# Performance work log

Hardware: AMD Instinct MI355X
Metric: run time of the kernel (lower is better)

The kernel has to match this reference:

```python
import jax, jax.numpy as jnp
import numpy as np

N_HEAD = 16
TEMPERATURE = 1.0

def setup_inputs() -> dict:
    key = jax.random.key(0)
    ks = jax.random.split(key, 5)
    B, L, D = 2, 2048, 1024
    s = 0.02
    return {
        'x':     jax.random.normal(ks[0], (B, L, D), jnp.float32),
        'q_g':   jax.random.normal(ks[1], (B, L, D), jnp.float32),
        'k_g':   jax.random.normal(ks[2], (B, L, D), jnp.float32),
        'W_qkv': jax.random.normal(ks[3], (D, 3 * D), jnp.float32) * s,
        'W_out': jax.random.normal(ks[4], (D, D), jnp.float32) * s,
    }

def reference(x, q_g, k_g, W_qkv, W_out):
    B, L, D = x.shape
    H = N_HEAD
    hd = D // H
    qkv = x @ W_qkv                                    # [B, L, 3D]
    q, k, v = jnp.split(qkv, 3, axis=-1)
    def to_heads(t):                                    # [B,L,D] -> [B,H,L,hd]
        return t.reshape(B, L, H, hd).transpose(0, 2, 1, 3)
    q, k, v = to_heads(q), to_heads(k), to_heads(v)
    qg, kg = to_heads(q_g), to_heads(k_g)

    scale = 1.0 / jnp.sqrt(jnp.float32(hd))
    # dual score matrices (same math as concat-on-head-dim then split)
    aw_x = jnp.einsum('bhqd,bhkd->bhqk', q, k) * scale    # [B,H,L,L]
    aw_g = jnp.einsum('bhqd,bhkd->bhqk', qg, kg) * scale  # [B,H,L,L]
    # sensory_attention=True, merge='add'
    attn = aw_x + aw_g

    causal = jnp.tril(jnp.ones((L, L), dtype=bool))
    attn = jnp.where(causal, attn, -jnp.inf)
    log_norm = jnp.log(jnp.float32(L))                    # softmax_log_norm=True
    attn = jax.nn.softmax(attn / (log_norm * TEMPERATURE), axis=-1)

    y = jnp.einsum('bhqk,bhkd->bhqd', attn, v)            # [B,H,L,hd]
    y = y.transpose(0, 2, 1, 3).reshape(B, L, D)
    return y @ W_out
```

## Files before the change

kernel.cpp:

```cpp
#include <hip/hip_runtime.h>
#include <type_traits>

typedef __attribute__((ext_vector_type(8))) short bf16x8;
typedef __attribute__((ext_vector_type(4))) float f32x4;

static __device__ __forceinline__ unsigned short f2bf(float f) {
    unsigned int u = __float_as_uint(f);
    u += 0x7fffu + ((u >> 16) & 1u);
    return (unsigned short)(u >> 16);
}
static __device__ __forceinline__ unsigned short f2bf_fast(float f) {
    return (unsigned short)((__float_as_uint(f) + 0x8000u) >> 16);
}

static __device__ __forceinline__ float bf2f(short v) {
    return __uint_as_float(((unsigned int)(unsigned short)v) << 16);
}

static __device__ __forceinline__ bf16x8 cvt8v(const float* p) {
    f32x4 a = *(const f32x4*)p, b = *(const f32x4*)(p + 4);
    bf16x8 r;
    r[0] = (short)f2bf(a[0]); r[1] = (short)f2bf(a[1]);
    r[2] = (short)f2bf(a[2]); r[3] = (short)f2bf(a[3]);
    r[4] = (short)f2bf(b[0]); r[5] = (short)f2bf(b[1]);
    r[6] = (short)f2bf(b[2]); r[7] = (short)f2bf(b[3]);
    return r;
}
static __device__ __forceinline__ bf16x8 scale8v(bf16x8 v, float s) {
    bf16x8 r;
    #pragma unroll
    for (int j = 0; j < 8; ++j) r[j] = (short)f2bf(bf2f(v[j]) * s);
    return r;
}
static __device__ __forceinline__ uint4 cvt8(const float* p) {
    bf16x8 r = cvt8v(p);
    union { bf16x8 v; uint4 u; } c; c.v = r; return c.u;
}

static __device__ __forceinline__ void glds16(const unsigned short* g, unsigned short* l) {
    __builtin_amdgcn_global_load_lds(
        (const __attribute__((address_space(1))) unsigned int*)g,
        (__attribute__((address_space(3))) unsigned int*)l, 16, 0, 0);
}

__global__ __launch_bounds__(256) void cvt_bf16(
    const float* __restrict__ src, unsigned short* __restrict__ dst, int n8)
{
    int i = blockIdx.x * 256 + threadIdx.x;
    if (i < n8) *(uint4*)&dst[(size_t)i * 8] = cvt8(&src[(size_t)i * 8]);
}

__global__ __launch_bounds__(256) void transpose_cvt(
    const float* __restrict__ src, unsigned short* __restrict__ dst, int R, int C)
{
    __shared__ unsigned short t[64 * 72];
    const int r0 = blockIdx.y * 64, c0 = blockIdx.x * 64;
    const int tid = threadIdx.x;
    #pragma unroll
    for (int i = 0; i < 4; ++i) {
        int idx = tid + i * 256;
        int row = idx >> 4, seg = idx & 15;
        f32x4 v = *(const f32x4*)&src[(size_t)(r0 + row) * C + c0 + seg * 4];
        #pragma unroll
        for (int j = 0; j < 4; ++j) t[row * 72 + seg * 4 + j] = f2bf(v[j]);
    }
    __syncthreads();
    #pragma unroll
    for (int i = 0; i < 2; ++i) {
        int idx = tid + i * 256;
        int row = idx >> 3, seg = idx & 7;
        uint4 tv; unsigned short* tmp = (unsigned short*)&tv;
        #pragma unroll
        for (int j = 0; j < 8; ++j) tmp[j] = t[(seg * 8 + j) * 72 + row];
        *(uint4*)&dst[(size_t)(c0 + row) * R + r0 + seg * 8] = tv;
    }
}

__global__ __launch_bounds__(256) void transpose_v(
    const unsigned short* __restrict__ qkv, unsigned short* __restrict__ vt)
{
    __shared__ unsigned short t[64 * 72];
    const int lt = blockIdx.x, bh = blockIdx.y, b = bh >> 4, h = bh & 15;
    const int tid = threadIdx.x;
    #pragma unroll
    for (int i = 0; i < 2; ++i) {
        int idx = tid + i * 256, row = idx >> 3, seg = idx & 7;
        *(uint4*)&t[row * 72 + seg * 8] =
            *(const uint4*)&qkv[(size_t)(b * 2048 + lt * 64 + row) * 3072 + 2048 + h * 64 + seg * 8];
    }
    __syncthreads();
    #pragma unroll
    for (int i = 0; i < 2; ++i) {
        int idx = tid + i * 256, row = idx >> 3, seg = idx & 7;
        uint4 tv; unsigned short* tmp = (unsigned short*)&tv;
        #pragma unroll
        for (int j = 0; j < 8; ++j) tmp[j] = t[(seg * 8 + j) * 72 + row];
        *(uint4*)&vt[((size_t)bh * 64 + row) * 2048 + lt * 64 + seg * 8] = tv;
    }
}

template <typename OT>
__global__ __launch_bounds__(256) void gemm_lds(
    const unsigned short* __restrict__ A, const unsigned short* __restrict__ Bt,
    OT* __restrict__ C, int M, int N, int K)
{
    __shared__ unsigned short As[128 * 32];
    __shared__ unsigned short Bs[128 * 32];
    const int tid = threadIdx.x;
    const int wave = tid >> 6, lane = tid & 63, quad = lane >> 4, l16 = lane & 15;
    const int wr = (wave >> 1) * 64, wc = (wave & 1) * 64;
    const int m0 = blockIdx.y * 128, n0 = blockIdx.x * 128;

    const unsigned short* ga = A  + (size_t)(m0 + wave * 32 + (lane >> 2)) * K + (lane & 3) * 8;
    const unsigned short* gb = Bt + (size_t)(n0 + wave * 32 + (lane >> 2)) * K + (lane & 3) * 8;
    unsigned short* la = &As[wave * 32 * 32];
    unsigned short* lb = &Bs[wave * 32 * 32];
    const size_t step16 = (size_t)16 * K;

    f32x4 acc[4][4];
    #pragma unroll
    for (int i = 0; i < 4; ++i)
        #pragma unroll
        for (int j = 0; j < 4; ++j) acc[i][j] = (f32x4){0.f, 0.f, 0.f, 0.f};

    for (int kt = 0; kt < K; kt += 32) {
        glds16(ga, la);
        glds16(ga + step16, la + 512);
        glds16(gb, lb);
        glds16(gb + step16, lb + 512);
        ga += 32; gb += 32;
        __syncthreads();
        bf16x8 af[4], bf[4];
        #pragma unroll
        for (int i = 0; i < 4; ++i) {
            af[i] = *(const bf16x8*)&As[(wr + i * 16 + l16) * 32 + quad * 8];
            bf[i] = *(const bf16x8*)&Bs[(wc + i * 16 + l16) * 32 + quad * 8];
        }
        #pragma unroll
        for (int mi = 0; mi < 4; ++mi)
            #pragma unroll
            for (int ni = 0; ni < 4; ++ni)
                acc[mi][ni] = __builtin_amdgcn_mfma_f32_16x16x32_bf16(
                    af[mi], bf[ni], acc[mi][ni], 0, 0, 0);
        __syncthreads();
    }
    #pragma unroll
    for (int mi = 0; mi < 4; ++mi)
        #pragma unroll
        for (int ni = 0; ni < 4; ++ni)
            #pragma unroll
            for (int r = 0; r < 4; ++r) {
                int row = m0 + wr + mi * 16 + quad * 4 + r;
                int col = n0 + wc + ni * 16 + l16;
                if constexpr (std::is_same_v<OT, float>)
                    C[(size_t)row * N + col] = acc[mi][ni][r];
                else
                    C[(size_t)row * N + col] = f2bf(acc[mi][ni][r]);
            }
}

__global__ __launch_bounds__(256, 4) void attn5(
    const unsigned short* __restrict__ qkv, const float* __restrict__ qg,
    const unsigned short* __restrict__ kgb, const unsigned short* __restrict__ vt,
    unsigned short* __restrict__ y)
{
    const int L = 2048, D3 = 3072, Dm = 1024;
    const float SC2 = 0.125f * 1.44269504088896f / 7.6246189861593985f;

    const int qt = 31 - (int)blockIdx.y;
    const int bh = blockIdx.x, b = bh >> 4, h = bh & 15;
    const int tid = threadIdx.x, wave = tid >> 6, lane = tid & 63;
    const int quad = lane >> 4, l16 = lane & 15;

    __shared__ unsigned short K_l[4096];
    __shared__ unsigned short G_l[4096];
    __shared__ unsigned short V_l[4096];
    __shared__ unsigned short P_l[4 * 1152];
    unsigned short* Pw = &P_l[wave * 1152];

    bf16x8 qf[2], gf[2];
    {
        const int qrow = qt * 64 + wave * 16 + l16;
        const unsigned short* qp = qkv + (size_t)(b * L + qrow) * D3 + h * 64;
        const float* gp = qg + (size_t)(b * L + qrow) * Dm + h * 64;
        #pragma unroll
        for (int c = 0; c < 2; ++c) {
            qf[c] = scale8v(*(const bf16x8*)(qp + c * 32 + quad * 8), SC2);
            gf[c] = scale8v(cvt8v(gp + c * 32 + quad * 8), SC2);
        }
    }

    f32x4 o[4];
    #pragma unroll
    for (int nd = 0; nd < 4; ++nd) o[nd] = (f32x4){0.f, 0.f, 0.f, 0.f};
    float lsum[4];
    #pragma unroll
    for (int r = 0; r < 4; ++r) lsum[r] = 0.f;

    const int srow = wave * 16 + (lane >> 3);
    const int c8 = (((lane & 7) ^ (lane >> 3)) & 7) * 8;
    const unsigned short* pk = qkv + (size_t)(b * L + srow) * D3 + 1024 + h * 64 + c8;
    const unsigned short* pg = kgb + (size_t)(b * L + srow) * Dm + h * 64 + c8;
    const unsigned short* pv = vt + ((size_t)bh * 64 + srow) * L + c8;
    unsigned short* lK = &K_l[wave * 1024];
    unsigned short* lG = &G_l[wave * 1024];
    unsigned short* lV = &V_l[wave * 1024];

    const int rb = l16 * 128;
    const int swz0 = ((quad     ^ (l16 & 7)) * 16);
    const int swz1 = (((4 + quad) ^ (l16 & 7)) * 16);

    const int ktmax = qt;
    for (int kt = 0; kt <= ktmax; ++kt) {
        __syncthreads();
        glds16(pk, lK); glds16(pk + 8 * D3, lK + 512);
        glds16(pg, lG); glds16(pg + 8 * Dm, lG + 512);
        glds16(pv, lV); glds16(pv + 8 * L,  lV + 512);
        pk += 64 * D3; pg += 64 * Dm; pv += 64;
        __syncthreads();

        f32x4 s[4];
        #pragma unroll
        for (int ni = 0; ni < 4; ++ni) {
            bf16x8 kf0 = *(const bf16x8*)((const char*)K_l + rb + swz0 + ni * 2048);
            bf16x8 kf1 = *(const bf16x8*)((const char*)K_l + rb + swz1 + ni * 2048);
            bf16x8 gb0 = *(const bf16x8*)((const char*)G_l + rb + swz0 + ni * 2048);
            bf16x8 gb1 = *(const bf16x8*)((const char*)G_l + rb + swz1 + ni * 2048);
            f32x4 a = (f32x4){0.f, 0.f, 0.f, 0.f};
            a = __builtin_amdgcn_mfma_f32_16x16x32_bf16(qf[0], kf0, a, 0, 0, 0);
            a = __builtin_amdgcn_mfma_f32_16x16x32_bf16(gf[0], gb0, a, 0, 0, 0);
            a = __builtin_amdgcn_mfma_f32_16x16x32_bf16(qf[1], kf1, a, 0, 0, 0);
            a = __builtin_amdgcn_mfma_f32_16x16x32_bf16(gf[1], gb1, a, 0, 0, 0);
            s[ni] = a;
        }

        {
            const int rowbase = qt * 64 + wave * 16 + quad * 4;
            const bool safe = (kt * 64 + 63 <= rowbase);
            #pragma unroll
            for (int ni = 0; ni < 4; ++ni) {
                const int key = kt * 64 + ni * 16 + l16;
                #pragma unroll
                for (int r = 0; r < 4; ++r) {
                    float e = (safe || key <= rowbase + r) ? exp2f(s[ni][r]) : 0.f;
                    lsum[r] += e;
                    Pw[(quad * 4 + r) * 72 + ni * 16 + l16] = f2bf_fast(e);
                }
            }
        }
        asm volatile("s_waitcnt lgkmcnt(0)" ::: "memory");

        bf16x8 pa[2];
        #pragma unroll
        for (int c = 0; c < 2; ++c)
            pa[c] = *(const bf16x8*)&Pw[l16 * 72 + c * 32 + quad * 8];
        #pragma unroll
        for (int nd = 0; nd < 4; ++nd) {
            bf16x8 vf0 = *(const bf16x8*)((const char*)V_l + rb + swz0 + nd * 2048);
            bf16x8 vf1 = *(const bf16x8*)((const char*)V_l + rb + swz1 + nd * 2048);
            o[nd] = __builtin_amdgcn_mfma_f32_16x16x32_bf16(pa[0], vf0, o[nd], 0, 0, 0);
            o[nd] = __builtin_amdgcn_mfma_f32_16x16x32_bf16(pa[1], vf1, o[nd], 0, 0, 0);
        }
    }

    #pragma unroll
    for (int r = 0; r < 4; ++r) {
        float rs = lsum[r];
        #pragma unroll
        for (int off = 1; off < 16; off <<= 1) rs += __shfl_xor(rs, off);
        float inv = 1.f / rs;
        int row = qt * 64 + wave * 16 + quad * 4 + r;
        #pragma unroll
        for (int nd = 0; nd < 4; ++nd)
            y[(size_t)(b * L + row) * Dm + h * 64 + nd * 16 + l16] =
                f2bf(o[nd][r] * inv);
    }
}

extern "C" void kernel_launch(void* const* d_in, const int* in_sizes, int n_in,
                              void* d_out, int out_size, void* d_ws, size_t ws_size,
                              hipStream_t stream) {
    const float* x     = (const float*)d_in[0];
    const float* q_g   = (const float*)d_in[1];
    const float* k_g   = (const float*)d_in[2];
    const float* W_qkv = (const float*)d_in[3];
    const float* W_out = (const float*)d_in[4];
    float* out = (float*)d_out;
    unsigned short* ws = (unsigned short*)d_ws;

    unsigned short* qkv_ws = ws;
    unsigned short* y_ws   = ws + 12582912;
    unsigned short* wtq    = ws + 16777216;
    unsigned short* wto    = ws + 19922944;
    unsigned short* kg_bf  = ws + 20971520;
    unsigned short* x_bf   = ws + 25165824;
    unsigned short* vt_bf  = x_bf;

    dim3 blk(256);
    cvt_bf16<<<2048, blk, 0, stream>>>(x,   x_bf,  524288);
    cvt_bf16<<<2048, blk, 0, stream>>>(k_g, kg_bf, 524288);
    transpose_cvt<<<dim3(48, 16), blk, 0, stream>>>(W_qkv, wtq, 1024, 3072);
    transpose_cvt<<<dim3(16, 16), blk, 0, stream>>>(W_out, wto, 1024, 1024);
    gemm_lds<unsigned short><<<dim3(24, 32), blk, 0, stream>>>(
        x_bf, wtq, qkv_ws, 4096, 3072, 1024);
    transpose_v<<<dim3(32, 32), blk, 0, stream>>>(qkv_ws, vt_bf);
    attn5<<<dim3(32, 32), blk, 0, stream>>>(qkv_ws, q_g, kg_bf, vt_bf, y_ws);
    gemm_lds<float><<<dim3(8, 32), blk, 0, stream>>>(
        y_ws, wto, out, 4096, 1024, 1024);
}
```

Before: 235.2 us.

## Peel diagonal tile, transpose score MFMA, pack P stores, merge convert launches

```diff
diff --git a/kernel.cpp b/kernel.cpp
--- a/kernel.cpp
+++ b/kernel.cpp
@@ -9,8 +9,9 @@
     u += 0x7fffu + ((u >> 16) & 1u);
     return (unsigned short)(u >> 16);
 }
-static __device__ __forceinline__ unsigned short f2bf_fast(float f) {
-    return (unsigned short)((__float_as_uint(f) + 0x8000u) >> 16);
+static __device__ __forceinline__ unsigned int pack2bf(float lo, float hi) {
+    return ((__float_as_uint(lo) + 0x8000u) >> 16) |
+           ((__float_as_uint(hi) + 0x8000u) & 0xffff0000u);
 }
 
 static __device__ __forceinline__ float bf2f(short v) {
@@ -43,11 +44,15 @@
         (__attribute__((address_space(3))) unsigned int*)l, 16, 0, 0);
 }
 
-__global__ __launch_bounds__(256) void cvt_bf16(
-    const float* __restrict__ src, unsigned short* __restrict__ dst, int n8)
+__global__ __launch_bounds__(256) void cvt_bf16_2(
+    const float* __restrict__ a, unsigned short* __restrict__ da,
+    const float* __restrict__ b, unsigned short* __restrict__ db)
 {
     int i = blockIdx.x * 256 + threadIdx.x;
-    if (i < n8) *(uint4*)&dst[(size_t)i * 8] = cvt8(&src[(size_t)i * 8]);
+    const float* s = (i < 524288) ? a : b;
+    unsigned short* d = (i < 524288) ? da : db;
+    size_t j = (size_t)((i < 524288) ? i : i - 524288) * 8;
+    *(uint4*)&d[j] = cvt8(&s[j]);
 }
 
 __global__ __launch_bounds__(256) void transpose_cvt(
@@ -159,7 +164,7 @@
             }
 }
 
-__global__ __launch_bounds__(256, 4) void attn5(
+__global__ __launch_bounds__(256, 4) void attn6(
     const unsigned short* __restrict__ qkv, const float* __restrict__ qg,
     const unsigned short* __restrict__ kgb, const unsigned short* __restrict__ vt,
     unsigned short* __restrict__ y)
@@ -193,9 +198,7 @@
     f32x4 o[4];
     #pragma unroll
     for (int nd = 0; nd < 4; ++nd) o[nd] = (f32x4){0.f, 0.f, 0.f, 0.f};
-    float lsum[4];
-    #pragma unroll
-    for (int r = 0; r < 4; ++r) lsum[r] = 0.f;
+    float lsum = 0.f;
 
     const int srow = wave * 16 + (lane >> 3);
     const int c8 = (((lane & 7) ^ (lane >> 3)) & 7) * 8;
@@ -210,8 +213,7 @@
     const int swz0 = ((quad     ^ (l16 & 7)) * 16);
     const int swz1 = (((4 + quad) ^ (l16 & 7)) * 16);
 
-    const int ktmax = qt;
-    for (int kt = 0; kt <= ktmax; ++kt) {
+    for (int kt = 0; kt < qt; ++kt) {
         __syncthreads();
         glds16(pk, lK); glds16(pk + 8 * D3, lK + 512);
         glds16(pg, lG); glds16(pg + 8 * Dm, lG + 512);
@@ -219,7 +221,6 @@
         pk += 64 * D3; pg += 64 * Dm; pv += 64;
         __syncthreads();
 
-        f32x4 s[4];
         #pragma unroll
         for (int ni = 0; ni < 4; ++ni) {
             bf16x8 kf0 = *(const bf16x8*)((const char*)K_l + rb + swz0 + ni * 2048);
@@ -227,26 +228,16 @@
             bf16x8 gb0 = *(const bf16x8*)((const char*)G_l + rb + swz0 + ni * 2048);
             bf16x8 gb1 = *(const bf16x8*)((const char*)G_l + rb + swz1 + ni * 2048);
             f32x4 a = (f32x4){0.f, 0.f, 0.f, 0.f};
-            a = __builtin_amdgcn_mfma_f32_16x16x32_bf16(qf[0], kf0, a, 0, 0, 0);
-            a = __builtin_amdgcn_mfma_f32_16x16x32_bf16(gf[0], gb0, a, 0, 0, 0);
-            a = __builtin_amdgcn_mfma_f32_16x16x32_bf16(qf[1], kf1, a, 0, 0, 0);
-            a = __builtin_amdgcn_mfma_f32_16x16x32_bf16(gf[1], gb1, a, 0, 0, 0);
-            s[ni] = a;
-        }
-
-        {
-            const int rowbase = qt * 64 + wave * 16 + quad * 4;
-            const bool safe = (kt * 64 + 63 <= rowbase);
-            #pragma unroll
-            for (int ni = 0; ni < 4; ++ni) {
-                const int key = kt * 64 + ni * 16 + l16;
-                #pragma unroll
-                for (int r = 0; r < 4; ++r) {
-                    float e = (safe || key <= rowbase + r) ? exp2f(s[ni][r]) : 0.f;
-                    lsum[r] += e;
-                    Pw[(quad * 4 + r) * 72 + ni * 16 + l16] = f2bf_fast(e);
-                }
-            }
+            a = __builtin_amdgcn_mfma_f32_16x16x32_bf16(kf0, qf[0], a, 0, 0, 0);
+            a = __builtin_amdgcn_mfma_f32_16x16x32_bf16(gb0, gf[0], a, 0, 0, 0);
+            a = __builtin_amdgcn_mfma_f32_16x16x32_bf16(kf1, qf[1], a, 0, 0, 0);
+            a = __builtin_amdgcn_mfma_f32_16x16x32_bf16(gb1, gf[1], a, 0, 0, 0);
+            float e0 = exp2f(a[0]), e1 = exp2f(a[1]);
+            float e2 = exp2f(a[2]), e3 = exp2f(a[3]);
+            lsum += (e0 + e1) + (e2 + e3);
+            unsigned int p01 = pack2bf(e0, e1), p23 = pack2bf(e2, e3);
+            *(unsigned long long*)&Pw[l16 * 72 + ni * 16 + quad * 4] =
+                ((unsigned long long)p23 << 32) | p01;
         }
         asm volatile("s_waitcnt lgkmcnt(0)" ::: "memory");
 
@@ -263,12 +254,64 @@
         }
     }
 
+    {
+        __syncthreads();
+        glds16(pk, lK); glds16(pk + 8 * D3, lK + 512);
+        glds16(pg, lG); glds16(pg + 8 * Dm, lG + 512);
+        glds16(pv, lV); glds16(pv + 8 * L,  lV + 512);
+        __syncthreads();
+
+        #pragma unroll
+        for (int ni = 0; ni < 4; ++ni) {
+            if (ni > wave) {
+                *(unsigned long long*)&Pw[l16 * 72 + ni * 16 + quad * 4] = 0ull;
+                continue;
+            }
+            bf16x8 kf0 = *(const bf16x8*)((const char*)K_l + rb + swz0 + ni * 2048);
+            bf16x8 kf1 = *(const bf16x8*)((const char*)K_l + rb + swz1 + ni * 2048);
+            bf16x8 gb0 = *(const bf16x8*)((const char*)G_l + rb + swz0 + ni * 2048);
+            bf16x8 gb1 = *(const bf16x8*)((const char*)G_l + rb + swz1 + ni * 2048);
+            f32x4 a = (f32x4){0.f, 0.f, 0.f, 0.f};
+            a = __builtin_amdgcn_mfma_f32_16x16x32_bf16(kf0, qf[0], a, 0, 0, 0);
+            a = __builtin_amdgcn_mfma_f32_16x16x32_bf16(gb0, gf[0], a, 0, 0, 0);
+            a = __builtin_amdgcn_mfma_f32_16x16x32_bf16(kf1, qf[1], a, 0, 0, 0);
+            a = __builtin_amdgcn_mfma_f32_16x16x32_bf16(gb1, gf[1], a, 0, 0, 0);
+            float e0, e1, e2, e3;
+            if (ni < wave) {
+                e0 = exp2f(a[0]); e1 = exp2f(a[1]);
+                e2 = exp2f(a[2]); e3 = exp2f(a[3]);
+            } else {
+                e0 = (quad * 4 + 0 <= l16) ? exp2f(a[0]) : 0.f;
+                e1 = (quad * 4 + 1 <= l16) ? exp2f(a[1]) : 0.f;
+                e2 = (quad * 4 + 2 <= l16) ? exp2f(a[2]) : 0.f;
+                e3 = (quad * 4 + 3 <= l16) ? exp2f(a[3]) : 0.f;
+            }
+            lsum += (e0 + e1) + (e2 + e3);
+            unsigned int p01 = pack2bf(e0, e1), p23 = pack2bf(e2, e3);
+            *(unsigned long long*)&Pw[l16 * 72 + ni * 16 + quad * 4] =
+                ((unsigned long long)p23 << 32) | p01;
+        }
+        asm volatile("s_waitcnt lgkmcnt(0)" ::: "memory");
+
+        bf16x8 pa[2];
+        #pragma unroll
+        for (int c = 0; c < 2; ++c)
+            pa[c] = *(const bf16x8*)&Pw[l16 * 72 + c * 32 + quad * 8];
+        #pragma unroll
+        for (int nd = 0; nd < 4; ++nd) {
+            bf16x8 vf0 = *(const bf16x8*)((const char*)V_l + rb + swz0 + nd * 2048);
+            bf16x8 vf1 = *(const bf16x8*)((const char*)V_l + rb + swz1 + nd * 2048);
+            o[nd] = __builtin_amdgcn_mfma_f32_16x16x32_bf16(pa[0], vf0, o[nd], 0, 0, 0);
+            o[nd] = __builtin_amdgcn_mfma_f32_16x16x32_bf16(pa[1], vf1, o[nd], 0, 0, 0);
+        }
+    }
+
+    float rs = lsum;
+    rs += __shfl_xor(rs, 16);
+    rs += __shfl_xor(rs, 32);
     #pragma unroll
     for (int r = 0; r < 4; ++r) {
-        float rs = lsum[r];
-        #pragma unroll
-        for (int off = 1; off < 16; off <<= 1) rs += __shfl_xor(rs, off);
-        float inv = 1.f / rs;
+        float inv = 1.f / __shfl(rs, (lane & 48) | (quad * 4 + r));
         int row = qt * 64 + wave * 16 + quad * 4 + r;
         #pragma unroll
         for (int nd = 0; nd < 4; ++nd)
@@ -297,14 +340,13 @@
     unsigned short* vt_bf  = x_bf;
 
     dim3 blk(256);
-    cvt_bf16<<<2048, blk, 0, stream>>>(x,   x_bf,  524288);
-    cvt_bf16<<<2048, blk, 0, stream>>>(k_g, kg_bf, 524288);
+    cvt_bf16_2<<<4096, blk, 0, stream>>>(x, x_bf, k_g, kg_bf);
     transpose_cvt<<<dim3(48, 16), blk, 0, stream>>>(W_qkv, wtq, 1024, 3072);
     transpose_cvt<<<dim3(16, 16), blk, 0, stream>>>(W_out, wto, 1024, 1024);
     gemm_lds<unsigned short><<<dim3(24, 32), blk, 0, stream>>>(
         x_bf, wtq, qkv_ws, 4096, 3072, 1024);
     transpose_v<<<dim3(32, 32), blk, 0, stream>>>(qkv_ws, vt_bf);
-    attn5<<<dim3(32, 32), blk, 0, stream>>>(qkv_ws, q_g, kg_bf, vt_bf, y_ws);
+    attn6<<<dim3(32, 32), blk, 0, stream>>>(qkv_ws, q_g, kg_bf, vt_bf, y_ws);
     gemm_lds<float><<<dim3(8, 32), blk, 0, stream>>>(
         y_ws, wto, out, 4096, 1024, 1024);
 }
```

Result: no change. 233.3 us (-0.8%).
